# Optimization experiments

Measured on AMD Instinct MI355X. Metric: run time of the kernel, lower is better.

The kernel has to match this reference:

```python
import jax, jax.numpy as jnp
import numpy as np
from jax import lax

C = 64      # embed_dim
DI = 128    # d_inner (expand=2)
N = 16      # d_state
RK = 4      # dt_rank = ceil(C/16)
K = 4       # scan directions
NB = 8      # total VSS blocks (4 stages x 2)


def conv2d(x, w, b, stride=1, pad=1, groups=1):
    y = lax.conv_general_dilated(x, w, (stride, stride), [(pad, pad), (pad, pad)],
                                 dimension_numbers=('NCHW', 'OIHW', 'NCHW'),
                                 feature_group_count=groups)
    return y + b[None, :, None, None]


def ln2d(x, g, b, eps=1e-6):
    xt = x.transpose(0, 2, 3, 1)
    mu = xt.mean(-1, keepdims=True)
    var = ((xt - mu) ** 2).mean(-1, keepdims=True)
    y = (xt - mu) / jnp.sqrt(var + eps) * g + b
    return y.transpose(0, 3, 1, 2)


def selective_scan(u, delta, A, Bm, Cm, D):
    # u, delta: (B,K,d,L); A: (K,d,n); Bm, Cm: (B,K,n,L); D: (K,d)
    dA = jnp.exp(delta[..., None] * A[None, :, :, None, :])               # (B,K,d,L,n)
    dBu = delta[..., None] * Bm.transpose(0, 1, 3, 2)[:, :, None] * u[..., None]

    def comb(c1, c2):
        a1, b1 = c1
        a2, b2 = c2
        return a2 * a1, a2 * b1 + b2

    _, h = lax.associative_scan(comb, (dA, dBu), axis=3)                  # (B,K,d,L,n)
    y = jnp.einsum('bkdln,bkln->bkdl', h, Cm.transpose(0, 1, 3, 2))
    return y + D[None, :, :, None] * u


def vss_block(x, lg, lb, inw, cw, cb, xpw, dtw, dtb, a_log, dp, ong, onb, outw):
    B, _, H, W = x.shape
    L = H * W
    h = ln2d(x, lg, lb)
    xz = jnp.einsum('bchw,ce->behw', h, inw)                              # (B,2*DI,H,W)
    xc, z = xz[:, :DI], xz[:, DI:]
    xc = jax.nn.silu(conv2d(xc, cw, cb, groups=DI))                       # depthwise 3x3
    x1 = xc.reshape(B, DI, L)                                             # row-major
    x2 = xc.transpose(0, 1, 3, 2).reshape(B, DI, L)                       # col-major
    xs = jnp.stack([x1, x2, x1[..., ::-1], x2[..., ::-1]], axis=1)        # (B,K,DI,L)
    xdbl = jnp.einsum('bkdl,krd->bkrl', xs, xpw)
    dts, Bs, Cs = xdbl[:, :, :RK], xdbl[:, :, RK:RK + N], xdbl[:, :, RK + N:]
    delta = jax.nn.softplus(jnp.einsum('bkrl,kdr->bkdl', dts, dtw) + dtb[None, :, :, None])
    A = -jnp.exp(a_log)
    ys = selective_scan(xs, delta, A, Bs, Cs, dp)                         # (B,K,DI,L)
    y = (ys[:, 0].reshape(B, DI, H, W)
         + ys[:, 1].reshape(B, DI, W, H).transpose(0, 1, 3, 2)
         + ys[:, 2, :, ::-1].reshape(B, DI, H, W)
         + ys[:, 3, :, ::-1].reshape(B, DI, W, H).transpose(0, 1, 3, 2))
    yt = y.transpose(0, 2, 3, 1)
    mu = yt.mean(-1, keepdims=True)
    var = ((yt - mu) ** 2).mean(-1, keepdims=True)
    yt = (yt - mu) / jnp.sqrt(var + 1e-6) * ong + onb
    yt = yt * jax.nn.silu(z.transpose(0, 2, 3, 1))
    out = jnp.einsum('bhwd,dc->bhwc', yt, outw).transpose(0, 3, 1, 2)
    return x + out


def setup_inputs() -> dict:
    key = jax.random.key(0)
    ks = jax.random.split(key, 16)
    nrm = lambda k, s, sc=0.02: jax.random.normal(k, s, jnp.float32) * sc
    return dict(
        E0=jax.random.uniform(ks[0], (1, 1, 256, 256), jnp.float32),
        pe_w=nrm(ks[1], (C, 1, 4, 4), 0.1),
        pe_b=jnp.zeros((C,), jnp.float32),
        pe_lg=jnp.ones((C,), jnp.float32),
        pe_lb=jnp.zeros((C,), jnp.float32),
        ln_g=jnp.ones((NB, C), jnp.float32),
        ln_b=jnp.zeros((NB, C), jnp.float32),
        in_w=nrm(ks[2], (NB, C, 2 * DI)),
        cv_w=nrm(ks[3], (NB, DI, 1, 3, 3), 0.1),
        cv_b=jnp.zeros((NB, DI), jnp.float32),
        xp_w=nrm(ks[4], (NB, K, RK + 2 * N, DI)),
        dt_w=nrm(ks[5], (NB, K, DI, RK)),
        dt_b=nrm(ks[6], (NB, K, DI), 0.5),
        A_log=jnp.broadcast_to(jnp.log(jnp.arange(1., N + 1)), (NB, K, DI, N)).astype(jnp.float32),
        Dp=jnp.ones((NB, K, DI), jnp.float32),
        on_g=jnp.ones((NB, DI), jnp.float32),
        on_b=jnp.zeros((NB, DI), jnp.float32),
        out_pw=nrm(ks[7], (NB, DI, C)),
        dn_w=nrm(ks[8], (3, C, C, 3, 3), 0.05),
        dn_b=jnp.zeros((3, C), jnp.float32),
        dn_g=jnp.ones((3, C), jnp.float32),
        dn_lb=jnp.zeros((3, C), jnp.float32),
        up_w=nrm(ks[9], (3, C, C, 3, 3), 0.05),
        up_b=jnp.zeros((3, C), jnp.float32),
        oc_w=nrm(ks[10], (C, C, 3, 3), 0.05),
        oc_b=jnp.zeros((C,), jnp.float32),
    )


def reference(E0, pe_w, pe_b, pe_lg, pe_lb, ln_g, ln_b, in_w, cv_w, cv_b, xp_w,
              dt_w, dt_b, A_log, Dp, on_g, on_b, out_pw, dn_w, dn_b, dn_g, dn_lb,
              up_w, up_b, oc_w, oc_b):
    x = conv2d(E0, pe_w, pe_b, stride=4, pad=0)
    x = ln2d(x, pe_lg, pe_lb)
    skips = []
    cur = 0
    for i in range(4):
        for _ in range(2):
            x = vss_block(x, ln_g[cur], ln_b[cur], in_w[cur], cv_w[cur], cv_b[cur],
                          xp_w[cur], dt_w[cur], dt_b[cur], A_log[cur], Dp[cur],
                          on_g[cur], on_b[cur], out_pw[cur])
            cur += 1
        skips.append(x)
        if i < 3:
            x = ln2d(conv2d(x, dn_w[i], dn_b[i], stride=2), dn_g[i], dn_lb[i])
    for i in range(3):
        Bq, Cq, Hq, Wq = x.shape
        x = jax.image.resize(x, (Bq, Cq, Hq * 2, Wq * 2), method='bilinear')
        x = jax.nn.silu(conv2d(x, up_w[i], up_b[i]))
        x = x + skips[-(i + 2)]
    Bq, Cq, Hq, Wq = x.shape
    x = jax.image.resize(x, (Bq, Cq, Hq * 4, Wq * 4), method='bilinear')
    x = jax.nn.silu(conv2d(x, oc_w, oc_b))
    return x
```

## Files before the change

### kernel.cpp

```cpp
#include <hip/hip_runtime.h>
#include <hip/hip_bf16.h>
#include <utility>

#define CIC 8

__global__ void k_patch_embed_ln(const float* __restrict__ E0, const float* __restrict__ w,
                                 const float* __restrict__ b, const float* __restrict__ g,
                                 const float* __restrict__ lb, float* __restrict__ out) {
  int p = blockIdx.x;
  int c = threadIdx.x;
  int oh = p >> 6, ow = p & 63;
  const float* src = E0 + (oh * 4) * 256 + ow * 4;
  const float* wc = w + c * 16;
  float acc = b[c];
#pragma unroll
  for (int i = 0; i < 4; i++)
#pragma unroll
    for (int j = 0; j < 4; j++) acc += src[i * 256 + j] * wc[i * 4 + j];
  float s = acc, s2 = acc * acc;
#pragma unroll
  for (int m = 32; m >= 1; m >>= 1) {
    s += __shfl_xor(s, m, 64);
    s2 += __shfl_xor(s2, m, 64);
  }
  float mu = s * (1.f / 64.f);
  float var = s2 * (1.f / 64.f) - mu * mu;
  float rstd = rsqrtf(var + 1e-6f);
  out[c * 4096 + p] = (acc - mu) * rstd * g[c] + lb[c];
}

__global__ void k_ln2d64(const float* __restrict__ x, const float* __restrict__ g,
                         const float* __restrict__ b, float* __restrict__ y, int HW) {
  int p = blockIdx.x;
  int c = threadIdx.x;
  float v = x[c * HW + p];
  float s = v, s2 = v * v;
#pragma unroll
  for (int m = 32; m >= 1; m >>= 1) {
    s += __shfl_xor(s, m, 64);
    s2 += __shfl_xor(s2, m, 64);
  }
  float mu = s * (1.f / 64.f);
  float var = s2 * (1.f / 64.f) - mu * mu;
  float rstd = rsqrtf(var + 1e-6f);
  y[c * HW + p] = (v - mu) * rstd * g[c] + b[c];
}

__global__ void k_lnproj(const float* __restrict__ x, const float* __restrict__ g,
                         const float* __restrict__ b, const float* __restrict__ w,
                         float* __restrict__ xc, float* __restrict__ z, int HW) {
  int p = blockIdx.x;
  int t = threadIdx.x;
  __shared__ float hsh[64];
  if (t < 64) {
    float v = x[t * HW + p];
    float s = v, s2 = v * v;
#pragma unroll
    for (int m = 32; m >= 1; m >>= 1) {
      s += __shfl_xor(s, m, 64);
      s2 += __shfl_xor(s2, m, 64);
    }
    float mu = s * (1.f / 64.f);
    float var = s2 * (1.f / 64.f) - mu * mu;
    float rstd = rsqrtf(var + 1e-6f);
    hsh[t] = (v - mu) * rstd * g[t] + b[t];
  }
  __syncthreads();
  float acc = 0.f;
  const float* wp = w + t;
#pragma unroll
  for (int c = 0; c < 64; c++) acc += hsh[c] * wp[c * 256];
  if (t < 128)
    xc[(size_t)p * 128 + t] = acc;
  else
    z[(size_t)p * 128 + (t - 128)] = acc;
}

__global__ void k_dwconv(const float* __restrict__ xc, const float* __restrict__ w,
                         const float* __restrict__ b, float* __restrict__ out, int H, int lgH) {
  int HW = H * H;
  int idx = blockIdx.x * blockDim.x + threadIdx.x;
  if (idx >= 128 * HW) return;
  int p = idx >> 7;
  int d = idx & 127;
  int ph = p >> lgH, pw = p & (H - 1);
  const float* wp = w + d * 9;
  float acc = b[d];
#pragma unroll
  for (int i = 0; i < 3; i++) {
    int ih = ph + i - 1;
    if (ih < 0 || ih >= H) continue;
#pragma unroll
    for (int j = 0; j < 3; j++) {
      int iw = pw + j - 1;
      if (iw < 0 || iw >= H) continue;
      acc += xc[(size_t)(ih * H + iw) * 128 + d] * wp[i * 3 + j];
    }
  }
  out[(size_t)p * 128 + d] = acc / (1.f + __expf(-acc));
}

__global__ void k_xproj(const float* __restrict__ xcs, const float* __restrict__ xpw,
                        const float* __restrict__ dtw, const float* __restrict__ dtb,
                        float* __restrict__ delta, float* __restrict__ Bs,
                        float* __restrict__ Cs, int H, int lgH) {
  int L = H * H;
  int l = blockIdx.x;
  int k = blockIdx.y;
  int t = threadIdx.x;
  int lm = (k & 2) ? (L - 1 - l) : l;
  int idx = (k & 1) ? ((lm & (H - 1)) * H + (lm >> lgH)) : lm;
  __shared__ float xs[128];
  __shared__ float part[36][4];
  __shared__ float r4[4];
  if (t < 128) xs[t] = xcs[(size_t)idx * 128 + t];
  __syncthreads();
  if (t < 144) {
    int r = t >> 2, q = t & 3;
    const float* wr = xpw + (k * 36 + r) * 128 + q * 32;
    const float* xp = xs + q * 32;
    float acc = 0.f;
#pragma unroll
    for (int c = 0; c < 32; c++) acc += xp[c] * wr[c];
    part[r][q] = acc;
  }
  __syncthreads();
  if (t < 36) {
    float acc = part[t][0] + part[t][1] + part[t][2] + part[t][3];
    if (t < 4)
      r4[t] = acc;
    else if (t < 20)
      Bs[((size_t)k * L + l) * 16 + (t - 4)] = acc;
    else
      Cs[((size_t)k * L + l) * 16 + (t - 20)] = acc;
  }
  __syncthreads();
  if (t < 128) {
    float dt = dtb[k * 128 + t];
    const float* wd = dtw + (k * 128 + t) * 4;
    dt += r4[0] * wd[0] + r4[1] * wd[1] + r4[2] * wd[2] + r4[3] * wd[3];
    float sp = fmaxf(dt, 0.f) + log1pf(__expf(-fabsf(dt)));
    delta[((size_t)k * L + l) * 128 + t] = sp;
  }
}

__global__ void k_scanA(const float* __restrict__ xcs, const float* __restrict__ delta,
                        const float* __restrict__ Bs, const float* __restrict__ A_log,
                        float* __restrict__ hloc, float* __restrict__ pA, int H, int lgH,
                        int nc, int cs) {
  int L = H * H;
  int c = blockIdx.x;
  int k = blockIdx.y;
  int d = threadIdx.x;
  float A[16], h[16];
#pragma unroll
  for (int n = 0; n < 16; n++) {
    A[n] = -expf(A_log[(k * 128 + d) * 16 + n]);
    h[n] = 0.f;
  }
  float sumdt = 0.f;
  int l0 = c * cs;
  for (int l = l0; l < l0 + cs; l++) {
    int lm = (k & 2) ? (L - 1 - l) : l;
    int idx = (k & 1) ? ((lm & (H - 1)) * H + (lm >> lgH)) : lm;
    float u = xcs[(size_t)idx * 128 + d];
    float dt = delta[((size_t)k * L + l) * 128 + d];
    float du = dt * u;
    sumdt += dt;
    const float4* bp = (const float4*)(Bs + ((size_t)k * L + l) * 16);
    float4 B0 = bp[0], B1 = bp[1], B2 = bp[2], B3 = bp[3];
    float Bv[16] = {B0.x, B0.y, B0.z, B0.w, B1.x, B1.y, B1.z, B1.w,
                    B2.x, B2.y, B2.z, B2.w, B3.x, B3.y, B3.z, B3.w};
#pragma unroll
    for (int n = 0; n < 16; n++) h[n] = __expf(dt * A[n]) * h[n] + Bv[n] * du;
  }
  size_t base = (((size_t)(k * 128 + d)) * nc + c) * 16;
#pragma unroll
  for (int n = 0; n < 16; n++) {
    hloc[base + n] = h[n];
    pA[base + n] = __expf(A[n] * sumdt);
  }
}

__global__ void k_scanB(const float* __restrict__ hloc, const float* __restrict__ pA,
                        float* __restrict__ hinit, int nc) {
  int tid = blockIdx.x * blockDim.x + threadIdx.x;
  int k = tid >> 11;
  int d = (tid >> 4) & 127;
  int n = tid & 15;
  size_t rb = ((size_t)(k * 128 + d)) * nc * 16 + n;
  float h = 0.f;
  for (int c = 0; c < nc; c++) {
    size_t a = rb + (size_t)c * 16;
    hinit[a] = h;
    h = pA[a] * h + hloc[a];
  }
}

__global__ void k_scanC(const float* __restrict__ xcs, const float* __restrict__ delta,
                        const float* __restrict__ Bs, const float* __restrict__ Cs,
                        const float* __restrict__ A_log, const float* __restrict__ Dp,
                        const float* __restrict__ hinit, float* __restrict__ ys, int H,
                        int lgH, int nc, int cs) {
  int L = H * H;
  int c = blockIdx.x;
  int k = blockIdx.y;
  int d = threadIdx.x;
  float A[16], h[16];
  size_t base = (((size_t)(k * 128 + d)) * nc + c) * 16;
#pragma unroll
  for (int n = 0; n < 16; n++) {
    A[n] = -expf(A_log[(k * 128 + d) * 16 + n]);
    h[n] = hinit[base + n];
  }
  float Dv = Dp[k * 128 + d];
  int l0 = c * cs;
  for (int l = l0; l < l0 + cs; l++) {
    int lm = (k & 2) ? (L - 1 - l) : l;
    int idx = (k & 1) ? ((lm & (H - 1)) * H + (lm >> lgH)) : lm;
    float u = xcs[(size_t)idx * 128 + d];
    float dt = delta[((size_t)k * L + l) * 128 + d];
    float du = dt * u;
    const float4* bp = (const float4*)(Bs + ((size_t)k * L + l) * 16);
    float4 B0 = bp[0], B1 = bp[1], B2 = bp[2], B3 = bp[3];
    float Bv[16] = {B0.x, B0.y, B0.z, B0.w, B1.x, B1.y, B1.z, B1.w,
                    B2.x, B2.y, B2.z, B2.w, B3.x, B3.y, B3.z, B3.w};
    const float4* cp = (const float4*)(Cs + ((size_t)k * L + l) * 16);
    float4 C0 = cp[0], C1 = cp[1], C2 = cp[2], C3 = cp[3];
    float Cv[16] = {C0.x, C0.y, C0.z, C0.w, C1.x, C1.y, C1.z, C1.w,
                    C2.x, C2.y, C2.z, C2.w, C3.x, C3.y, C3.z, C3.w};
    float y = 0.f;
#pragma unroll
    for (int n = 0; n < 16; n++) {
      h[n] = __expf(dt * A[n]) * h[n] + Bv[n] * du;
      y += h[n] * Cv[n];
    }
    ys[((size_t)k * L + l) * 128 + d] = y + Dv * u;
  }
}

__global__ void __launch_bounds__(1024) k_scan_fused(
    const float* __restrict__ xcs, const float* __restrict__ delta,
    const float* __restrict__ Bs, const float* __restrict__ Cs,
    const float* __restrict__ A_log, const float* __restrict__ Dp,
    float* __restrict__ hloc, float* __restrict__ pA, float* __restrict__ hinit,
    float* __restrict__ ys, int H, int lgH, int nc) {
  const int cs = 8;
  int L = H * H;
  int k = blockIdx.x;
  for (int item = threadIdx.x; item < nc * 128; item += 1024) {
    int c = item >> 7, d = item & 127;
    float A[16], h[16];
#pragma unroll
    for (int n = 0; n < 16; n++) {
      A[n] = -expf(A_log[(k * 128 + d) * 16 + n]);
      h[n] = 0.f;
    }
    float sumdt = 0.f;
    int l0 = c * cs;
    for (int l = l0; l < l0 + cs; l++) {
      int lm = (k & 2) ? (L - 1 - l) : l;
      int idx = (k & 1) ? ((lm & (H - 1)) * H + (lm >> lgH)) : lm;
      float u = xcs[(size_t)idx * 128 + d];
      float dt = delta[((size_t)k * L + l) * 128 + d];
      float du = dt * u;
      sumdt += dt;
      const float4* bp = (const float4*)(Bs + ((size_t)k * L + l) * 16);
      float4 B0 = bp[0], B1 = bp[1], B2 = bp[2], B3 = bp[3];
      float Bv[16] = {B0.x, B0.y, B0.z, B0.w, B1.x, B1.y, B1.z, B1.w,
                      B2.x, B2.y, B2.z, B2.w, B3.x, B3.y, B3.z, B3.w};
#pragma unroll
      for (int n = 0; n < 16; n++) h[n] = __expf(dt * A[n]) * h[n] + Bv[n] * du;
    }
    size_t base = (((size_t)(k * 128 + d)) * nc + c) * 16;
#pragma unroll
    for (int n = 0; n < 16; n++) {
      hloc[base + n] = h[n];
      pA[base + n] = __expf(A[n] * sumdt);
    }
  }
  __syncthreads();
  for (int item = threadIdx.x; item < 2048; item += 1024) {
    int d = item >> 4, n = item & 15;
    size_t rb = ((size_t)(k * 128 + d)) * nc * 16 + n;
    float h = 0.f;
    for (int c = 0; c < nc; c++) {
      size_t a = rb + (size_t)c * 16;
      hinit[a] = h;
      h = pA[a] * h + hloc[a];
    }
  }
  __syncthreads();
  for (int item = threadIdx.x; item < nc * 128; item += 1024) {
    int c = item >> 7, d = item & 127;
    float A[16], h[16];
    size_t base = (((size_t)(k * 128 + d)) * nc + c) * 16;
#pragma unroll
    for (int n = 0; n < 16; n++) {
      A[n] = -expf(A_log[(k * 128 + d) * 16 + n]);
      h[n] = hinit[base + n];
    }
    float Dv = Dp[k * 128 + d];
    int l0 = c * cs;
    for (int l = l0; l < l0 + cs; l++) {
      int lm = (k & 2) ? (L - 1 - l) : l;
      int idx = (k & 1) ? ((lm & (H - 1)) * H + (lm >> lgH)) : lm;
      float u = xcs[(size_t)idx * 128 + d];
      float dt = delta[((size_t)k * L + l) * 128 + d];
      float du = dt * u;
      const float4* bp = (const float4*)(Bs + ((size_t)k * L + l) * 16);
      float4 B0 = bp[0], B1 = bp[1], B2 = bp[2], B3 = bp[3];
      float Bv[16] = {B0.x, B0.y, B0.z, B0.w, B1.x, B1.y, B1.z, B1.w,
                      B2.x, B2.y, B2.z, B2.w, B3.x, B3.y, B3.z, B3.w};
      const float4* cp = (const float4*)(Cs + ((size_t)k * L + l) * 16);
      float4 C0 = cp[0], C1 = cp[1], C2 = cp[2], C3 = cp[3];
      float Cv[16] = {C0.x, C0.y, C0.z, C0.w, C1.x, C1.y, C1.z, C1.w,
                      C2.x, C2.y, C2.z, C2.w, C3.x, C3.y, C3.z, C3.w};
      float y = 0.f;
#pragma unroll
      for (int n = 0; n < 16; n++) {
        h[n] = __expf(dt * A[n]) * h[n] + Bv[n] * du;
        y += h[n] * Cv[n];
      }
      ys[((size_t)k * L + l) * 128 + d] = y + Dv * u;
    }
  }
}

__global__ void k_combine(const float* __restrict__ ys, const float* __restrict__ z,
                          const float* __restrict__ xin, const float* __restrict__ ong,
                          const float* __restrict__ onb, const float* __restrict__ outw,
                          float* __restrict__ xout, int H, int lgH) {
  int L = H * H;
  int p = blockIdx.x;
  int d = threadIdx.x;
  int ph = p >> lgH, pw = p & (H - 1);
  int l1 = pw * H + ph;
  float yv = ys[((size_t)0 * L + p) * 128 + d] + ys[((size_t)1 * L + l1) * 128 + d] +
             ys[((size_t)2 * L + (L - 1 - p)) * 128 + d] +
             ys[((size_t)3 * L + (L - 1 - l1)) * 128 + d];
  float s = yv, s2 = yv * yv;
#pragma unroll
  for (int m = 32; m >= 1; m >>= 1) {
    s += __shfl_xor(s, m, 64);
    s2 += __shfl_xor(s2, m, 64);
  }
  __shared__ float ws1[2], ws2[2];
  int wid = d >> 6;
  if ((d & 63) == 0) {
    ws1[wid] = s;
    ws2[wid] = s2;
  }
  __syncthreads();
  float tot = ws1[0] + ws1[1], tot2 = ws2[0] + ws2[1];
  float mu = tot * (1.f / 128.f);
  float var = tot2 * (1.f / 128.f) - mu * mu;
  float rstd = rsqrtf(var + 1e-6f);
  float zt = z[(size_t)p * 128 + d];
  float yt = ((yv - mu) * rstd * ong[d] + onb[d]) * (zt / (1.f + __expf(-zt)));
  __shared__ float ysm[128];
  ysm[d] = yt;
  __syncthreads();
  if (d < 64) {
    float acc = xin[(size_t)d * L + p];
#pragma unroll
    for (int q = 0; q < 128; q++) acc += ysm[q] * outw[q * 64 + d];
    xout[(size_t)d * L + p] = acc;
  }
}

__global__ void k_combine_lnproj(const float* __restrict__ ys, const float* __restrict__ z,
                                 const float* __restrict__ xin, const float* __restrict__ ong,
                                 const float* __restrict__ onb, const float* __restrict__ outw,
                                 const float* __restrict__ g2, const float* __restrict__ b2,
                                 const float* __restrict__ w2, float* __restrict__ xout,
                                 float* __restrict__ xc, float* __restrict__ zout, int H,
                                 int lgH) {
  int L = H * H;
  int p = blockIdx.x;
  int t = threadIdx.x;
  __shared__ float ysm[128], hnsh[64];
  __shared__ float ws1[2], ws2[2];
  float yv = 0.f;
  if (t < 128) {
    int ph = p >> lgH, pw = p & (H - 1);
    int l1 = pw * H + ph;
    yv = ys[((size_t)0 * L + p) * 128 + t] + ys[((size_t)1 * L + l1) * 128 + t] +
         ys[((size_t)2 * L + (L - 1 - p)) * 128 + t] +
         ys[((size_t)3 * L + (L - 1 - l1)) * 128 + t];
    float s = yv, s2 = yv * yv;
#pragma unroll
    for (int m = 32; m >= 1; m >>= 1) {
      s += __shfl_xor(s, m, 64);
      s2 += __shfl_xor(s2, m, 64);
    }
    if ((t & 63) == 0) {
      ws1[t >> 6] = s;
      ws2[t >> 6] = s2;
    }
  }
  __syncthreads();
  if (t < 128) {
    float tot = ws1[0] + ws1[1], tot2 = ws2[0] + ws2[1];
    float mu = tot * (1.f / 128.f);
    float var = tot2 * (1.f / 128.f) - mu * mu;
    float rstd = rsqrtf(var + 1e-6f);
    float zt = z[(size_t)p * 128 + t];
    ysm[t] = ((yv - mu) * rstd * ong[t] + onb[t]) * (zt / (1.f + __expf(-zt)));
  }
  __syncthreads();
  if (t < 64) {
    float acc = xin[(size_t)t * L + p];
#pragma unroll
    for (int q = 0; q < 128; q++) acc += ysm[q] * outw[q * 64 + t];
    xout[(size_t)t * L + p] = acc;
    float s = acc, s2 = acc * acc;
#pragma unroll
    for (int m = 32; m >= 1; m >>= 1) {
      s += __shfl_xor(s, m, 64);
      s2 += __shfl_xor(s2, m, 64);
    }
    float mu = s * (1.f / 64.f);
    float var = s2 * (1.f / 64.f) - mu * mu;
    float rstd = rsqrtf(var + 1e-6f);
    hnsh[t] = (acc - mu) * rstd * g2[t] + b2[t];
  }
  __syncthreads();
  float a2 = 0.f;
  const float* wp = w2 + t;
#pragma unroll
  for (int c = 0; c < 64; c++) a2 += hnsh[c] * wp[c * 256];
  if (t < 128)
    xc[(size_t)p * 128 + t] = a2;
  else
    zout[(size_t)p * 128 + (t - 128)] = a2;
}

__global__ void k_conv_naive(const float* __restrict__ x, const float* __restrict__ w,
                             const float* __restrict__ b, const float* __restrict__ skip,
                             float* __restrict__ out, int Hin, int Hout, int stride,
                             int do_silu) {
  int idx = blockIdx.x * blockDim.x + threadIdx.x;
  int HWo = Hout * Hout;
  if (idx >= 64 * HWo) return;
  int co = idx / HWo;
  int p = idx - co * HWo;
  int oh = p / Hout, ow = p - (p / Hout) * Hout;
  float acc = b[co];
  const float* wb = w + co * 64 * 9;
  for (int ci = 0; ci < 64; ci++) {
    const float* xb = x + (size_t)ci * Hin * Hin;
    const float* wc = wb + ci * 9;
#pragma unroll
    for (int i = 0; i < 3; i++) {
      int ih = oh * stride + i - 1;
      if (ih < 0 || ih >= Hin) continue;
#pragma unroll
      for (int j = 0; j < 3; j++) {
        int iw = ow * stride + j - 1;
        if (iw < 0 || iw >= Hin) continue;
        acc += xb[ih * Hin + iw] * wc[i * 3 + j];
      }
    }
  }
  if (do_silu) acc = acc / (1.f + __expf(-acc));
  if (skip) acc += skip[idx];
  out[idx] = acc;
}

__global__ void __launch_bounds__(256) k_conv16_up(const float* __restrict__ x,
                                                   const float* __restrict__ w,
                                                   const float* __restrict__ b,
                                                   float* __restrict__ out) {
  __shared__ __align__(16) float xsh[CIC][18][18];
  __shared__ __align__(16) float wsh[CIC][16][12];
  int t = threadIdx.x;
  int q = t & 63, cog = t >> 6;
  int qx = q & 7, qy = q >> 3;
  int ox = blockIdx.x * 16, oy = blockIdx.y * 16;
  int z16 = blockIdx.z * 16;
  float acc[4][4];
#pragma unroll
  for (int pp = 0; pp < 4; pp++)
#pragma unroll
    for (int i = 0; i < 4; i++) acc[pp][i] = 0.f;
  for (int cb = 0; cb < 64; cb += CIC) {
    for (int i = t; i < CIC * 324; i += 256) {
      int ci = i / 324;
      int r = i - ci * 324;
      int iy = r / 18, ix = r - (r / 18) * 18;
      int gy = oy + iy - 1, gx = ox + ix - 1;
      float v = 0.f;
      if (gy >= 0 && gy < 256 && gx >= 0 && gx < 256) {
        float sh = gy * 0.25f - 0.375f;
        float sw = gx * 0.25f - 0.375f;
        int h0 = (int)floorf(sh);
        float fh = sh - h0;
        int w0 = (int)floorf(sw);
        float fw = sw - w0;
        int h0c = max(h0, 0), h1c = min(h0 + 1, 63);
        int w0c = max(w0, 0), w1c = min(w0 + 1, 63);
        const float* xb = x + (size_t)(cb + ci) * 4096;
        v = (1.f - fh) * ((1.f - fw) * xb[h0c * 64 + w0c] + fw * xb[h0c * 64 + w1c]) +
            fh * ((1.f - fw) * xb[h1c * 64 + w0c] + fw * xb[h1c * 64 + w1c]);
      }
      xsh[ci][iy][ix] = v;
    }
    for (int i = t; i < CIC * 144; i += 256) {
      int ci = i / 144;
      int r = i - ci * 144;
      int col = r / 9, tap = r - (r / 9) * 9;
      wsh[ci][col][tap] = w[(size_t)(z16 + col) * 576 + (cb + ci) * 9 + tap];
    }
    __syncthreads();
#pragma unroll
    for (int ci = 0; ci < CIC; ci++) {
      float xv[4][4];
#pragma unroll
      for (int r = 0; r < 4; r++) {
        float2 a = *(const float2*)&xsh[ci][2 * qy + r][2 * qx];
        float2 bq = *(const float2*)&xsh[ci][2 * qy + r][2 * qx + 2];
        xv[r][0] = a.x;
        xv[r][1] = a.y;
        xv[r][2] = bq.x;
        xv[r][3] = bq.y;
      }
#pragma unroll
      for (int i = 0; i < 4; i++) {
        int col = cog * 4 + i;
        float4 w0 = *(const float4*)&wsh[ci][col][0];
        float4 w1 = *(const float4*)&wsh[ci][col][4];
        float w8 = wsh[ci][col][8];
#pragma unroll
        for (int dy = 0; dy < 2; dy++)
#pragma unroll
          for (int dx = 0; dx < 2; dx++) {
            acc[dy * 2 + dx][i] += xv[dy + 0][dx + 0] * w0.x + xv[dy + 0][dx + 1] * w0.y +
                                   xv[dy + 0][dx + 2] * w0.z + xv[dy + 1][dx + 0] * w0.w +
                                   xv[dy + 1][dx + 1] * w1.x + xv[dy + 1][dx + 2] * w1.y +
                                   xv[dy + 2][dx + 0] * w1.z + xv[dy + 2][dx + 1] * w1.w +
                                   xv[dy + 2][dx + 2] * w8;
          }
      }
    }
    __syncthreads();
  }
#pragma unroll
  for (int dy = 0; dy < 2; dy++)
#pragma unroll
    for (int dx = 0; dx < 2; dx++) {
      int gy = oy + 2 * qy + dy, gx = ox + 2 * qx + dx;
#pragma unroll
      for (int i = 0; i < 4; i++) {
        int co = z16 + cog * 4 + i;
        float a = acc[dy * 2 + dx][i] + b[co];
        a = a / (1.f + __expf(-a));
        out[(size_t)co * 65536 + gy * 256 + gx] = a;
      }
    }
}

__global__ void k_resize(const float* __restrict__ x, float* __restrict__ out, int Hin,
                         int Win, int Hout, int Wout, float inv_scale) {
  int idx = blockIdx.x * blockDim.x + threadIdx.x;
  int HWo = Hout * Wout;
  if (idx >= 64 * HWo) return;
  int c = idx / HWo;
  int p = idx - c * HWo;
  int oh = p / Wout, ow = p - (p / Wout) * Wout;
  float sh = (oh + 0.5f) * inv_scale - 0.5f;
  float sw = (ow + 0.5f) * inv_scale - 0.5f;
  int h0 = (int)floorf(sh);
  float fh = sh - h0;
  int w0 = (int)floorf(sw);
  float fw = sw - w0;
  int h0c = min(max(h0, 0), Hin - 1), h1c = min(max(h0 + 1, 0), Hin - 1);
  int w0c = min(max(w0, 0), Win - 1), w1c = min(max(w0 + 1, 0), Win - 1);
  const float* xb = x + (size_t)c * Hin * Win;
  float v = (1.f - fh) * ((1.f - fw) * xb[h0c * Win + w0c] + fw * xb[h0c * Win + w1c]) +
            fh * ((1.f - fw) * xb[h1c * Win + w0c] + fw * xb[h1c * Win + w1c]);
  out[idx] = v;
}

extern "C" void kernel_launch(void* const* d_in, const int* in_sizes, int n_in, void* d_out,
                              int out_size, void* d_ws, size_t ws_size, hipStream_t stream) {
  const float* E0 = (const float*)d_in[0];
  const float* pe_w = (const float*)d_in[1];
  const float* pe_b = (const float*)d_in[2];
  const float* pe_lg = (const float*)d_in[3];
  const float* pe_lb = (const float*)d_in[4];
  const float* ln_g = (const float*)d_in[5];
  const float* ln_b = (const float*)d_in[6];
  const float* in_w = (const float*)d_in[7];
  const float* cv_w = (const float*)d_in[8];
  const float* cv_b = (const float*)d_in[9];
  const float* xp_w = (const float*)d_in[10];
  const float* dt_w = (const float*)d_in[11];
  const float* dt_b = (const float*)d_in[12];
  const float* A_log = (const float*)d_in[13];
  const float* Dp = (const float*)d_in[14];
  const float* on_g = (const float*)d_in[15];
  const float* on_b = (const float*)d_in[16];
  const float* out_pw = (const float*)d_in[17];
  const float* dn_w = (const float*)d_in[18];
  const float* dn_b = (const float*)d_in[19];
  const float* dn_g = (const float*)d_in[20];
  const float* dn_lb = (const float*)d_in[21];
  const float* up_w = (const float*)d_in[22];
  const float* up_b = (const float*)d_in[23];
  const float* oc_w = (const float*)d_in[24];
  const float* oc_b = (const float*)d_in[25];

  float* ws = (float*)d_ws;
  size_t off = 0;
  auto alloc = [&](size_t n) {
    float* p = ws + off;
    off += n;
    return p;
  };
  float* xA = alloc(64 * 4096);
  float* xB = alloc(64 * 4096);
  float* xc = alloc(128 * 4096);
  float* zb = alloc(128 * 4096);
  float* xcs = alloc(128 * 4096);
  float* dlt = alloc((size_t)4 * 128 * 4096);
  float* Bsb = alloc(4 * 16 * 4096);
  float* Csb = alloc(4 * 16 * 4096);
  float* ysb = alloc((size_t)4 * 128 * 4096);
  float* hloc = alloc((size_t)4 * 128 * 256 * 16);
  float* pAb = alloc((size_t)4 * 128 * 256 * 16);
  float* hin = alloc((size_t)4 * 128 * 256 * 16);
  float* sk0 = alloc(64 * 4096);
  float* sk1 = alloc(64 * 1024);
  float* sk2 = alloc(64 * 256);
  float* sk3 = alloc(64 * 64);
  float* tmpR = alloc((size_t)64 * 4096);

  k_patch_embed_ln<<<4096, 64, 0, stream>>>(E0, pe_w, pe_b, pe_lg, pe_lb, xB);
  float* x = xB;
  float* xalt = xA;

  int Hs[4] = {64, 32, 16, 8};
  int lgHs[4] = {6, 5, 4, 3};
  int CSs[4] = {16, 8, 8, 8};
  float* skips[4] = {sk0, sk1, sk2, sk3};
  int cur = 0;

  auto vss_core = [&](int H, int lgH, int cs, bool fused_scan) {
    int L = H * H;
    int nc = L / cs;
    k_dwconv<<<(128 * L + 255) / 256, 256, 0, stream>>>(xc, cv_w + (size_t)cur * 128 * 9,
                                                        cv_b + cur * 128, xcs, H, lgH);
    dim3 gx(L, 4);
    k_xproj<<<gx, 256, 0, stream>>>(xcs, xp_w + (size_t)cur * 4 * 36 * 128,
                                    dt_w + (size_t)cur * 4 * 128 * 4, dt_b + cur * 4 * 128,
                                    dlt, Bsb, Csb, H, lgH);
    const float* Al = A_log + (size_t)cur * 4 * 128 * 16;
    const float* Dv = Dp + cur * 4 * 128;
    if (fused_scan) {
      k_scan_fused<<<4, 1024, 0, stream>>>(xcs, dlt, Bsb, Csb, Al, Dv, hloc, pAb, hin, ysb,
                                           H, lgH, nc);
    } else {
      dim3 ga(nc, 4);
      k_scanA<<<ga, 128, 0, stream>>>(xcs, dlt, Bsb, Al, hloc, pAb, H, lgH, nc, cs);
      k_scanB<<<32, 256, 0, stream>>>(hloc, pAb, hin, nc);
      k_scanC<<<ga, 128, 0, stream>>>(xcs, dlt, Bsb, Csb, Al, Dv, hin, ysb, H, lgH, nc, cs);
    }
  };

  for (int i = 0; i < 4; i++) {
    int H = Hs[i], lgH = lgHs[i];
    int L = H * H;
    bool fs = (i >= 2);
    k_lnproj<<<L, 256, 0, stream>>>(x, ln_g + cur * 64, ln_b + cur * 64,
                                    in_w + (size_t)cur * 64 * 256, xc, zb, L);
    vss_core(H, lgH, CSs[i], fs);
    k_combine_lnproj<<<L, 256, 0, stream>>>(
        ysb, zb, x, on_g + cur * 128, on_b + cur * 128, out_pw + (size_t)cur * 128 * 64,
        ln_g + (cur + 1) * 64, ln_b + (cur + 1) * 64, in_w + (size_t)(cur + 1) * 64 * 256,
        xalt, xc, zb, H, lgH);
    std::swap(x, xalt);
    cur++;
    vss_core(H, lgH, CSs[i], fs);
    k_combine<<<L, 128, 0, stream>>>(ysb, zb, x, on_g + cur * 128, on_b + cur * 128,
                                     out_pw + (size_t)cur * 128 * 64, xalt, H, lgH);
    std::swap(x, xalt);
    cur++;

    hipMemcpyAsync(skips[i], x, (size_t)64 * L * sizeof(float), hipMemcpyDeviceToDevice,
                   stream);
    if (i < 3) {
      int Ho = H / 2;
      k_conv_naive<<<(64 * Ho * Ho + 255) / 256, 256, 0, stream>>>(
          x, dn_w + (size_t)i * 64 * 64 * 9, dn_b + i * 64, nullptr, xalt, H, Ho, 2, 0);
      k_ln2d64<<<Ho * Ho, 64, 0, stream>>>(xalt, dn_g + i * 64, dn_lb + i * 64, x, Ho * Ho);
    }
  }

  for (int i = 0; i < 3; i++) {
    int Hin = 8 << i, Ho = Hin * 2;
    k_resize<<<(64 * Ho * Ho + 255) / 256, 256, 0, stream>>>(x, tmpR, Hin, Hin, Ho, Ho, 0.5f);
    k_conv_naive<<<(64 * Ho * Ho + 255) / 256, 256, 0, stream>>>(
        tmpR, up_w + (size_t)i * 64 * 64 * 9, up_b + i * 64, skips[2 - i], xalt, Ho, Ho, 1, 1);
    std::swap(x, xalt);
  }

  dim3 gf(16, 16, 4);
  k_conv16_up<<<gf, 256, 0, stream>>>(x, oc_w, oc_b, (float*)d_out);
}
```

Baseline: 1.508 ms.

## Drop fused single-block scan, enlarge scan chunks, widen conv tile, skip skip-copies

Removes the 4-block fused scan kernel and always uses the three-kernel chunked scan, with larger chunk sizes at the first two stages (fewer chunks, smaller carry buffers). Widens the final upsample conv's input-channel tile from 8 to 16 with padded shared rows to cut barrier rounds and bank conflicts. Writes the last combine of each stage directly into the skip buffer instead of a separate device copy. Longer chunks reduce parallelism at stage 0/1, and the shared memory footprint per block grows.

```diff
diff --git a/kernel.cpp b/kernel.cpp
--- a/kernel.cpp
+++ b/kernel.cpp
@@ -1,8 +1,6 @@
 #include <hip/hip_runtime.h>
 #include <hip/hip_bf16.h>
 #include <utility>
-
-#define CIC 8
 
 __global__ void k_patch_embed_ln(const float* __restrict__ E0, const float* __restrict__ w,
                                  const float* __restrict__ b, const float* __restrict__ g,
@@ -236,94 +234,6 @@
       y += h[n] * Cv[n];
     }
     ys[((size_t)k * L + l) * 128 + d] = y + Dv * u;
-  }
-}
-
-__global__ void __launch_bounds__(1024) k_scan_fused(
-    const float* __restrict__ xcs, const float* __restrict__ delta,
-    const float* __restrict__ Bs, const float* __restrict__ Cs,
-    const float* __restrict__ A_log, const float* __restrict__ Dp,
-    float* __restrict__ hloc, float* __restrict__ pA, float* __restrict__ hinit,
-    float* __restrict__ ys, int H, int lgH, int nc) {
-  const int cs = 8;
-  int L = H * H;
-  int k = blockIdx.x;
-  for (int item = threadIdx.x; item < nc * 128; item += 1024) {
-    int c = item >> 7, d = item & 127;
-    float A[16], h[16];
-#pragma unroll
-    for (int n = 0; n < 16; n++) {
-      A[n] = -expf(A_log[(k * 128 + d) * 16 + n]);
-      h[n] = 0.f;
-    }
-    float sumdt = 0.f;
-    int l0 = c * cs;
-    for (int l = l0; l < l0 + cs; l++) {
-      int lm = (k & 2) ? (L - 1 - l) : l;
-      int idx = (k & 1) ? ((lm & (H - 1)) * H + (lm >> lgH)) : lm;
-      float u = xcs[(size_t)idx * 128 + d];
-      float dt = delta[((size_t)k * L + l) * 128 + d];
-      float du = dt * u;
-      sumdt += dt;
-      const float4* bp = (const float4*)(Bs + ((size_t)k * L + l) * 16);
-      float4 B0 = bp[0], B1 = bp[1], B2 = bp[2], B3 = bp[3];
-      float Bv[16] = {B0.x, B0.y, B0.z, B0.w, B1.x, B1.y, B1.z, B1.w,
-                      B2.x, B2.y, B2.z, B2.w, B3.x, B3.y, B3.z, B3.w};
-#pragma unroll
-      for (int n = 0; n < 16; n++) h[n] = __expf(dt * A[n]) * h[n] + Bv[n] * du;
-    }
-    size_t base = (((size_t)(k * 128 + d)) * nc + c) * 16;
-#pragma unroll
-    for (int n = 0; n < 16; n++) {
-      hloc[base + n] = h[n];
-      pA[base + n] = __expf(A[n] * sumdt);
-    }
-  }
-  __syncthreads();
-  for (int item = threadIdx.x; item < 2048; item += 1024) {
-    int d = item >> 4, n = item & 15;
-    size_t rb = ((size_t)(k * 128 + d)) * nc * 16 + n;
-    float h = 0.f;
-    for (int c = 0; c < nc; c++) {
-      size_t a = rb + (size_t)c * 16;
-      hinit[a] = h;
-      h = pA[a] * h + hloc[a];
-    }
-  }
-  __syncthreads();
-  for (int item = threadIdx.x; item < nc * 128; item += 1024) {
-    int c = item >> 7, d = item & 127;
-    float A[16], h[16];
-    size_t base = (((size_t)(k * 128 + d)) * nc + c) * 16;
-#pragma unroll
-    for (int n = 0; n < 16; n++) {
-      A[n] = -expf(A_log[(k * 128 + d) * 16 + n]);
-      h[n] = hinit[base + n];
-    }
-    float Dv = Dp[k * 128 + d];
-    int l0 = c * cs;
-    for (int l = l0; l < l0 + cs; l++) {
-      int lm = (k & 2) ? (L - 1 - l) : l;
-      int idx = (k & 1) ? ((lm & (H - 1)) * H + (lm >> lgH)) : lm;
-      float u = xcs[(size_t)idx * 128 + d];
-      float dt = delta[((size_t)k * L + l) * 128 + d];
-      float du = dt * u;
-      const float4* bp = (const float4*)(Bs + ((size_t)k * L + l) * 16);
-      float4 B0 = bp[0], B1 = bp[1], B2 = bp[2], B3 = bp[3];
-      float Bv[16] = {B0.x, B0.y, B0.z, B0.w, B1.x, B1.y, B1.z, B1.w,
-                      B2.x, B2.y, B2.z, B2.w, B3.x, B3.y, B3.z, B3.w};
-      const float4* cp = (const float4*)(Cs + ((size_t)k * L + l) * 16);
-      float4 C0 = cp[0], C1 = cp[1], C2 = cp[2], C3 = cp[3];
-      float Cv[16] = {C0.x, C0.y, C0.z, C0.w, C1.x, C1.y, C1.z, C1.w,
-                      C2.x, C2.y, C2.z, C2.w, C3.x, C3.y, C3.z, C3.w};
-      float y = 0.f;
-#pragma unroll
-      for (int n = 0; n < 16; n++) {
-        h[n] = __expf(dt * A[n]) * h[n] + Bv[n] * du;
-        y += h[n] * Cv[n];
-      }
-      ys[((size_t)k * L + l) * 128 + d] = y + Dv * u;
-    }
   }
 }
 
@@ -472,8 +382,8 @@
                                                    const float* __restrict__ w,
                                                    const float* __restrict__ b,
                                                    float* __restrict__ out) {
-  __shared__ __align__(16) float xsh[CIC][18][18];
-  __shared__ __align__(16) float wsh[CIC][16][12];
+  __shared__ __align__(16) float xsh[16][18][20];
+  __shared__ __align__(16) float wsh[16][16][12];
   int t = threadIdx.x;
   int q = t & 63, cog = t >> 6;
   int qx = q & 7, qy = q >> 3;
@@ -484,14 +394,14 @@
   for (int pp = 0; pp < 4; pp++)
 #pragma unroll
     for (int i = 0; i < 4; i++) acc[pp][i] = 0.f;
-  for (int cb = 0; cb < 64; cb += CIC) {
-    for (int i = t; i < CIC * 324; i += 256) {
+  for (int cb = 0; cb < 64; cb += 16) {
+    for (int i = t; i < 16 * 324; i += 256) {
       int ci = i / 324;
       int r = i - ci * 324;
       int iy = r / 18, ix = r - (r / 18) * 18;
       int gy = oy + iy - 1, gx = ox + ix - 1;
       float v = 0.f;
-      if (gy >= 0 && gy < 256 && gx >= 0 && gx < 256) {
+      if ((unsigned)gy < 256u && (unsigned)gx < 256u) {
         float sh = gy * 0.25f - 0.375f;
         float sw = gx * 0.25f - 0.375f;
         int h0 = (int)floorf(sh);
@@ -506,7 +416,7 @@
       }
       xsh[ci][iy][ix] = v;
     }
-    for (int i = t; i < CIC * 144; i += 256) {
+    for (int i = t; i < 16 * 144; i += 256) {
       int ci = i / 144;
       int r = i - ci * 144;
       int col = r / 9, tap = r - (r / 9) * 9;
@@ -514,7 +424,7 @@
     }
     __syncthreads();
 #pragma unroll
-    for (int ci = 0; ci < CIC; ci++) {
+    for (int ci = 0; ci < 16; ci++) {
       float xv[4][4];
 #pragma unroll
       for (int r = 0; r < 4; r++) {
@@ -627,9 +537,9 @@
   float* Bsb = alloc(4 * 16 * 4096);
   float* Csb = alloc(4 * 16 * 4096);
   float* ysb = alloc((size_t)4 * 128 * 4096);
-  float* hloc = alloc((size_t)4 * 128 * 256 * 16);
-  float* pAb = alloc((size_t)4 * 128 * 256 * 16);
-  float* hin = alloc((size_t)4 * 128 * 256 * 16);
+  float* hloc = alloc((size_t)4 * 128 * 128 * 16);
+  float* pAb = alloc((size_t)4 * 128 * 128 * 16);
+  float* hin = alloc((size_t)4 * 128 * 128 * 16);
   float* sk0 = alloc(64 * 4096);
   float* sk1 = alloc(64 * 1024);
   float* sk2 = alloc(64 * 256);
@@ -642,11 +552,11 @@
 
   int Hs[4] = {64, 32, 16, 8};
   int lgHs[4] = {6, 5, 4, 3};
-  int CSs[4] = {16, 8, 8, 8};
+  int CSs[4] = {32, 16, 8, 8};
   float* skips[4] = {sk0, sk1, sk2, sk3};
   int cur = 0;
 
-  auto vss_core = [&](int H, int lgH, int cs, bool fused_scan) {
+  auto vss_core = [&](int H, int lgH, int cs) {
     int L = H * H;
     int nc = L / cs;
     k_dwconv<<<(128 * L + 255) / 256, 256, 0, stream>>>(xc, cv_w + (size_t)cur * 128 * 9,
@@ -657,43 +567,38 @@
                                     dlt, Bsb, Csb, H, lgH);
     const float* Al = A_log + (size_t)cur * 4 * 128 * 16;
     const float* Dv = Dp + cur * 4 * 128;
-    if (fused_scan) {
-      k_scan_fused<<<4, 1024, 0, stream>>>(xcs, dlt, Bsb, Csb, Al, Dv, hloc, pAb, hin, ysb,
-                                           H, lgH, nc);
-    } else {
-      dim3 ga(nc, 4);
-      k_scanA<<<ga, 128, 0, stream>>>(xcs, dlt, Bsb, Al, hloc, pAb, H, lgH, nc, cs);
-      k_scanB<<<32, 256, 0, stream>>>(hloc, pAb, hin, nc);
-      k_scanC<<<ga, 128, 0, stream>>>(xcs, dlt, Bsb, Csb, Al, Dv, hin, ysb, H, lgH, nc, cs);
-    }
+    dim3 ga(nc, 4);
+    k_scanA<<<ga, 128, 0, stream>>>(xcs, dlt, Bsb, Al, hloc, pAb, H, lgH, nc, cs);
+    k_scanB<<<32, 256, 0, stream>>>(hloc, pAb, hin, nc);
+    k_scanC<<<ga, 128, 0, stream>>>(xcs, dlt, Bsb, Csb, Al, Dv, hin, ysb, H, lgH, nc, cs);
   };
 
   for (int i = 0; i < 4; i++) {
     int H = Hs[i], lgH = lgHs[i];
     int L = H * H;
-    bool fs = (i >= 2);
     k_lnproj<<<L, 256, 0, stream>>>(x, ln_g + cur * 64, ln_b + cur * 64,
                                     in_w + (size_t)cur * 64 * 256, xc, zb, L);
-    vss_core(H, lgH, CSs[i], fs);
+    vss_core(H, lgH, CSs[i]);
     k_combine_lnproj<<<L, 256, 0, stream>>>(
         ysb, zb, x, on_g + cur * 128, on_b + cur * 128, out_pw + (size_t)cur * 128 * 64,
         ln_g + (cur + 1) * 64, ln_b + (cur + 1) * 64, in_w + (size_t)(cur + 1) * 64 * 256,
         xalt, xc, zb, H, lgH);
     std::swap(x, xalt);
     cur++;
-    vss_core(H, lgH, CSs[i], fs);
-    k_combine<<<L, 128, 0, stream>>>(ysb, zb, x, on_g + cur * 128, on_b + cur * 128,
-                                     out_pw + (size_t)cur * 128 * 64, xalt, H, lgH);
-    std::swap(x, xalt);
-    cur++;
-
-    hipMemcpyAsync(skips[i], x, (size_t)64 * L * sizeof(float), hipMemcpyDeviceToDevice,
-                   stream);
+    vss_core(H, lgH, CSs[i]);
     if (i < 3) {
+      k_combine<<<L, 128, 0, stream>>>(ysb, zb, x, on_g + cur * 128, on_b + cur * 128,
+                                       out_pw + (size_t)cur * 128 * 64, skips[i], H, lgH);
+      cur++;
       int Ho = H / 2;
       k_conv_naive<<<(64 * Ho * Ho + 255) / 256, 256, 0, stream>>>(
-          x, dn_w + (size_t)i * 64 * 64 * 9, dn_b + i * 64, nullptr, xalt, H, Ho, 2, 0);
+          skips[i], dn_w + (size_t)i * 64 * 64 * 9, dn_b + i * 64, nullptr, xalt, H, Ho, 2, 0);
       k_ln2d64<<<Ho * Ho, 64, 0, stream>>>(xalt, dn_g + i * 64, dn_lb + i * 64, x, Ho * Ho);
+    } else {
+      k_combine<<<L, 128, 0, stream>>>(ysb, zb, x, on_g + cur * 128, on_b + cur * 128,
+                                       out_pw + (size_t)cur * 128 * 64, xalt, H, lgH);
+      std::swap(x, xalt);
+      cur++;
     }
   }
 
```

After: 1.352 ms. 1.12x faster.
